# Kernel optimization log

Measured on AMD Instinct MI355X. Metric: run time of the kernel, lower is better.

Reference implementation:

```python
import jax, jax.numpy as jnp
import numpy as np

NH, KVH, HD = 32, 8, 128          # num heads, kv heads, head dim
HIDDEN = NH * HD                   # 4096
K_BITS = V_BITS = 4
GROUP = 32                         # quantization group size
THETA = 10000.0
FEAT = 32 // K_BITS                # values packed per int32


def _rope_cos_sin(pos, dtype=jnp.float32):
    inv_freq = 1.0 / (THETA ** (jnp.arange(0, HD, 2, dtype=jnp.float32) / HD))
    freqs = pos.astype(jnp.float32)[:, None] * inv_freq[None, :]
    emb = jnp.concatenate([freqs, freqs], axis=-1)  # [t, HD]
    return jnp.cos(emb).astype(dtype), jnp.sin(emb).astype(dtype)


def _rotate_half(x):
    x1, x2 = jnp.split(x, 2, axis=-1)
    return jnp.concatenate([-x2, x1], axis=-1)


def _apply_rope(x, pos):  # x: [b, h, t, d], pos: [t]
    cos, sin = _rope_cos_sin(pos, x.dtype)
    return x * cos[None, None] + _rotate_half(x) * sin[None, None]


def _unpack(packed, bits):
    # packed int32 [..., n] -> float [..., n * (32//bits)], little-endian bit fields
    feat = 32 // bits
    shifts = jnp.arange(feat, dtype=jnp.int32) * bits
    vals = (packed[..., None] >> shifts) & ((1 << bits) - 1)
    return vals.reshape(packed.shape[:-1] + (packed.shape[-1] * feat,)).astype(jnp.float32)


def _dequant(packed, scale, mn, bits, group):
    # group-wise affine dequant: x = q * scale + mn along last dim
    qv = _unpack(packed, bits)
    lead, L = qv.shape[:-1], qv.shape[-1]
    qv = qv.reshape(lead + (L // group, group))
    return (qv * scale[..., None] + mn[..., None]).reshape(lead + (L,))


def _repeat_kv(x, n):
    return jnp.repeat(x, n, axis=1)


def setup_inputs() -> dict:
    key = jax.random.key(0)
    ks = jax.random.split(key, 13)
    B, QL = 8, 8
    TQ, FULL_PAST = 3968, 56
    s = 0.02
    return {
        "hidden_states": jax.random.normal(ks[0], (B, QL, HIDDEN), jnp.float32),
        "Wq": jax.random.normal(ks[1], (NH * HD, HIDDEN), jnp.float32) * s,
        "Wk": jax.random.normal(ks[2], (KVH * HD, HIDDEN), jnp.float32) * s,
        "Wv": jax.random.normal(ks[3], (KVH * HD, HIDDEN), jnp.float32) * s,
        "Wo": jax.random.normal(ks[4], (NH * HD, NH * HD), jnp.float32) * s,
        "key_quant_trans": jax.random.randint(ks[5], (B, KVH, HD, TQ // FEAT), 0, 2**31 - 1, jnp.int32),
        "key_scale_trans": jax.random.uniform(ks[6], (B, KVH, HD, TQ // GROUP), jnp.float32) * 0.05 + 0.01,
        "key_mn_trans": jax.random.normal(ks[7], (B, KVH, HD, TQ // GROUP), jnp.float32) * 0.1,
        "key_full_past": jax.random.normal(ks[8], (B, KVH, FULL_PAST, HD), jnp.float32),
        "value_quant": jax.random.randint(ks[9], (B, KVH, TQ, HD // FEAT), 0, 2**31 - 1, jnp.int32),
        "value_scale": jax.random.uniform(ks[10], (B, KVH, TQ, HD // GROUP), jnp.float32) * 0.05 + 0.01,
        "value_mn": jax.random.normal(ks[11], (B, KVH, TQ, HD // GROUP), jnp.float32) * 0.1,
        "value_full_past": jax.random.normal(ks[12], (B, KVH, FULL_PAST, HD), jnp.float32),
    }


def reference(hidden_states, Wq, Wk, Wv, Wo,
              key_quant_trans, key_scale_trans, key_mn_trans, key_full_past,
              value_quant, value_scale, value_mn, value_full_past):
    b, q_len, _ = hidden_states.shape
    groups = NH // KVH
    # projections
    q = (hidden_states @ Wq.T).reshape(b, q_len, NH, HD).transpose(0, 2, 1, 3)
    k = (hidden_states @ Wk.T).reshape(b, q_len, KVH, HD).transpose(0, 2, 1, 3)
    v = (hidden_states @ Wv.T).reshape(b, q_len, KVH, HD).transpose(0, 2, 1, 3)

    TQ = key_quant_trans.shape[-1] * FEAT
    past_len = TQ + key_full_past.shape[2]
    pos_new = jnp.arange(past_len, past_len + q_len)
    qr = _apply_rope(q, pos_new)

    # quantized key segment: dequant (stored transposed [b,kvh,HD,TQ]) + fused RoPE + bmm
    kq = _dequant(key_quant_trans, key_scale_trans, key_mn_trans, K_BITS, GROUP)
    kq = _apply_rope(kq.transpose(0, 1, 3, 2), jnp.arange(TQ))  # [b,kvh,TQ,HD]
    att_quant = jnp.einsum('bhqd,bhkd->bhqk', qr, _repeat_kv(kq, groups))

    # full-precision residual key segment
    k_full = jnp.concatenate([key_full_past, k], axis=2)
    pos_full = jnp.arange(past_len + q_len - k_full.shape[2], past_len + q_len)
    k_full = _apply_rope(k_full, pos_full)
    att_full = jnp.einsum('bhqd,bhkd->bhqk', qr, _repeat_kv(k_full, groups))

    attn = jnp.concatenate([att_quant, att_full], axis=-1) / np.sqrt(HD).astype(np.float32)
    attn = jax.nn.softmax(attn.astype(jnp.float32), axis=-1).astype(qr.dtype)

    # quantized values (packed along head_dim) + full residual values
    vq = _dequant(value_quant, value_scale, value_mn, V_BITS, GROUP)  # [b,kvh,TQ,HD]
    v_full = jnp.concatenate([value_full_past, v], axis=2)
    Lf = v_full.shape[2]
    out = jnp.einsum('bhqk,bhkd->bhqd', attn[..., :-Lf], _repeat_kv(vq, groups)) \
        + jnp.einsum('bhqk,bhkd->bhqd', attn[..., -Lf:], _repeat_kv(v_full, groups))

    out = out.transpose(0, 2, 1, 3).reshape(b, q_len, NH * HD)
    return out @ Wo.T
```

## Files before the change

### kernel.cpp

```cpp
#include <hip/hip_runtime.h>

typedef unsigned short u16;
typedef short bf16x8 __attribute__((ext_vector_type(8)));
typedef float f32x4 __attribute__((ext_vector_type(4)));

__device__ __forceinline__ float b2f(u16 u){ return __uint_as_float(((unsigned)u)<<16); }
__device__ __forceinline__ u16 f2bf(float f){ return (u16)((__float_as_uint(f)+0x8000u)>>16); }
__device__ __forceinline__ float ldf(const void* p, int i, bool isbf){
  return isbf ? b2f(((const u16*)p)[i]) : ((const float*)p)[i];
}
__device__ __forceinline__ float2 ld2(const void* p, int i, bool isbf){
  if (isbf) { unsigned u = *(const unsigned*)((const u16*)p + i);
              return make_float2(b2f((u16)(u & 0xffffu)), b2f((u16)(u >> 16))); }
  return *(const float2*)((const float*)p + i);
}
__device__ __forceinline__ void ld8(u16* dst, const void* p, int i, bool isbf){
  if (isbf) { *(uint4*)dst = *(const uint4*)((const u16*)p + i); }
  else {
    float4 a = *(const float4*)((const float*)p + i);
    float4 b = *(const float4*)((const float*)p + i + 4);
    dst[0]=f2bf(a.x); dst[1]=f2bf(a.y); dst[2]=f2bf(a.z); dst[3]=f2bf(a.w);
    dst[4]=f2bf(b.x); dst[5]=f2bf(b.y); dst[6]=f2bf(b.z); dst[7]=f2bf(b.w);
  }
}
__device__ __forceinline__ void pre8(uint4& A, uint4& B, const void* p, int i, bool isb){
  if (isb) { A = *(const uint4*)((const u16*)p + i); }
  else { A = *(const uint4*)((const float*)p + i);
         B = *(const uint4*)((const float*)p + i + 4); }
}
__device__ __forceinline__ void st8(u16* dst, const uint4& A, const uint4& B, bool isb){
  if (isb) { *(uint4*)dst = A; }
  else {
    const float* a = (const float*)&A; const float* b = (const float*)&B;
    dst[0]=f2bf(a[0]); dst[1]=f2bf(a[1]); dst[2]=f2bf(a[2]); dst[3]=f2bf(a[3]);
    dst[4]=f2bf(b[0]); dst[5]=f2bf(b[1]); dst[6]=f2bf(b[2]); dst[7]=f2bf(b[3]);
  }
}
__device__ __forceinline__ float c8(const float* __restrict__ p, int i, int stride){
  float s = 0.f;
  #pragma unroll
  for (int k = 0; k < 8; k++) s += p[i + k*stride];
  return s;
}
__device__ __forceinline__ void bar(){ asm volatile("s_waitcnt lgkmcnt(0)\n\ts_barrier" ::: "memory"); }
#define RORMAX(x, ctrl) fmaxf((x), __int_as_float(__builtin_amdgcn_update_dpp( \
    __float_as_int(x), __float_as_int(x), (ctrl), 0xF, 0xF, false)))
#define MFMA16(a,b,c) __builtin_amdgcn_mfma_f32_16x16x32_bf16((a),(b),(c),0,0,0)

__global__ __launch_bounds__(256) void ctab_kernel(const u16* __restrict__ h,
                                                   int* __restrict__ flag,
                                                   float2* __restrict__ ctab) {
  int tid = threadIdx.x;
  if (blockIdx.x == 0) {
    int cnt = 0;
    for (int i = tid; i < 4096; i += 256) {
      int e = (h[i] >> 7) & 0xFF;
      cnt += (e >= 116 && e <= 132) ? 1 : 0;
    }
    __shared__ int sh[256];
    sh[tid] = cnt; __syncthreads();
    for (int s = 128; s > 0; s >>= 1) { if (tid < s) sh[tid] += sh[tid + s]; __syncthreads(); }
    if (tid == 0) flag[0] = (sh[0] >= 3100) ? 1 : 0;
  }
  int idx = blockIdx.x * 256 + tid;
  int dm = idx & 63, t = idx >> 6;
  float f = exp2f(-(float)dm * (13.287712379549449f / 64.0f));
  float ang = (float)t * f;
  float s, c;
  sincosf(ang, &s, &c);
  ctab[idx] = make_float2(c, s);
}

__global__ __launch_bounds__(256) void proj_kernel(
    const void* __restrict__ X, const void* __restrict__ Wa,
    const void* __restrict__ Wb, const void* __restrict__ Wc,
    float* __restrict__ out32, int Na, int Nb, int ostride,
    const int* __restrict__ flagp, int x_dyn)
{
  bool fbf = (*flagp != 0);
  bool xbf = x_dyn ? fbf : true;
  int n0 = blockIdx.x * 64;
  int ks0 = blockIdx.y * 512;
  const void* W; int wr0;
  if (n0 < Na)           { W = Wa; wr0 = n0; }
  else if (n0 < Na + Nb) { W = Wb; wr0 = n0 - Na; }
  else                   { W = Wc; wr0 = n0 - Na - Nb; }

  __shared__ u16 Xs[64][136];
  __shared__ u16 Ws[64][136];
  int tid = threadIdx.x;
  int wv = tid >> 6, lane = tid & 63, lr = lane & 15, lq = lane >> 4;
  f32x4 zf = {0.f,0.f,0.f,0.f};
  f32x4 acc[4] = {zf, zf, zf, zf};

  uint4 xa[4], xb[4], wa[4], wb[4];
  #pragma unroll
  for (int s = 0; s < 4; s++) {
    int e = s * 256 + tid, row = e >> 4, c8i = e & 15;
    pre8(xa[s], xb[s], X, row * 4096 + ks0 + c8i * 8, xbf);
    pre8(wa[s], wb[s], W, (wr0 + row) * 4096 + ks0 + c8i * 8, fbf);
  }
  #pragma unroll 1
  for (int ki = 0; ki < 4; ki++) {
    bar();
    #pragma unroll
    for (int s = 0; s < 4; s++) {
      int e = s * 256 + tid, row = e >> 4, c8i = e & 15;
      st8(&Xs[row][c8i * 8], xa[s], xb[s], xbf);
      st8(&Ws[row][c8i * 8], wa[s], wb[s], fbf);
    }
    if (ki < 3) {
      int k0 = ks0 + (ki + 1) * 128;
      #pragma unroll
      for (int s = 0; s < 4; s++) {
        int e = s * 256 + tid, row = e >> 4, c8i = e & 15;
        pre8(xa[s], xb[s], X, row * 4096 + k0 + c8i * 8, xbf);
        pre8(wa[s], wb[s], W, (wr0 + row) * 4096 + k0 + c8i * 8, fbf);
      }
    }
    bar();
    #pragma unroll
    for (int ks = 0; ks < 4; ks++) {
      bf16x8 af = *(const bf16x8*)&Xs[wv * 16 + lr][ks * 32 + lq * 8];
      #pragma unroll
      for (int nt = 0; nt < 4; nt++) {
        bf16x8 bv = *(const bf16x8*)&Ws[nt * 16 + lr][ks * 32 + lq * 8];
        acc[nt] = MFMA16(af, bv, acc[nt]);
      }
    }
  }
  float* outp = out32 + (size_t)blockIdx.y * 64 * ostride;
  #pragma unroll
  for (int nt = 0; nt < 4; nt++)
    #pragma unroll
    for (int r = 0; r < 4; r++)
      outp[(wv * 16 + lq * 4 + r) * ostride + n0 + nt * 16 + lr] = acc[nt][r];
}

__global__ __launch_bounds__(256) void prep_kernel(
    const float* __restrict__ Cq32, const void* __restrict__ kfp, const void* __restrict__ vfp,
    const float2* __restrict__ ctab, const int* __restrict__ flagp,
    u16* __restrict__ qrb, u16* __restrict__ kfullb, u16* __restrict__ vfullT)
{
  bool isbf = (*flagp != 0);
  int idx = blockIdx.x * 256 + threadIdx.x;
  if (idx < 262144) {
    int d = idx & 127, row = (idx >> 7) & 31, bh = idx >> 12;
    int b = bh >> 3, kvh = bh & 7, g = row >> 3, qp = row & 7;
    int tok = b * 8 + qp, h = kvh * 4 + g;
    float x  = c8(Cq32, tok * 6144 + h * 128 + d, 393216);
    float x2 = c8(Cq32, tok * 6144 + h * 128 + (d ^ 64), 393216);
    float2 cs = ctab[(4024 + qp) * 64 + (d & 63)];
    float sgn = (d < 64) ? -1.f : 1.f;
    qrb[idx] = f2bf(x * cs.x + sgn * (x2 * cs.y));
  } else if (idx < 786432) {
    int j = idx - 262144;
    int d = j & 127, t = (j >> 7) & 63, bh = j >> 13;
    int b = bh >> 3, kvh = bh & 7;
    float x, x2;
    if (t < 56) {
      x  = ldf(kfp, (bh * 56 + t) * 128 + d, isbf);
      x2 = ldf(kfp, (bh * 56 + t) * 128 + (d ^ 64), isbf);
    } else {
      int tok = b * 8 + (t - 56);
      x  = c8(Cq32, tok * 6144 + 4096 + kvh * 128 + d, 393216);
      x2 = c8(Cq32, tok * 6144 + 4096 + kvh * 128 + (d ^ 64), 393216);
    }
    float2 cs = ctab[(3968 + t) * 64 + (d & 63)];
    float sgn = (d < 64) ? -1.f : 1.f;
    kfullb[j] = f2bf(x * cs.x + sgn * (x2 * cs.y));
  } else {
    int j = idx - 786432;
    int t = j & 63, d = (j >> 6) & 127, bh = j >> 13;
    int b = bh >> 3, kvh = bh & 7;
    float x;
    if (t < 56) x = ldf(vfp, (bh * 56 + t) * 128 + d, isbf);
    else        x = c8(Cq32, (b * 8 + t - 56) * 6144 + 5120 + kvh * 128 + d, 393216);
    vfullT[j] = f2bf(x);
  }
}

__global__ __launch_bounds__(256) void attn_kernel(
    const int* __restrict__ kqw, const void* __restrict__ ksc, const void* __restrict__ kmn,
    const int* __restrict__ vqw, const void* __restrict__ vsc, const void* __restrict__ vmn,
    const u16* __restrict__ qrb, const u16* __restrict__ kfullb, const u16* __restrict__ vfullT,
    const float2* __restrict__ ctab, const int* __restrict__ flagp,
    u16* __restrict__ Opart, float* __restrict__ ml)
{
  bool isbf = (*flagp != 0);
  int bh = blockIdx.x, grp = blockIdx.y;
  int tid = threadIdx.x;
  int c0 = grp * 4;
  int N = (grp == 15) ? 3 : 4;

  __shared__ __align__(16) unsigned char L[37120];
  u16* Kt = (u16*)L;
  u16* Vt = (u16*)(L + 16384);
  u16* Pt = (u16*)(L + 32768);
  float* pmax = (float*)(L + 36864);

  int wv = tid >> 6, lane = tid & 63, lr = lane & 15, lq = lane >> 4;
  int mt = wv & 1, nh = wv >> 1;
  int sx = (lr & 7) << 3;

  const int* kq_lo = kqw + (bh * 128 + lane) * 496;
  const int* kq_hi = kq_lo + 64 * 496;
  int klo = (bh * 128 + lane) * 124;
  int khi = klo + 64 * 124;
  const int* vqp = vqw + (bh * 3968 + lane) * 16 + wv * 4;
  int voff = (bh * 3968 + lane) * 4 + wv;

  bf16x8 qa[4];
  #pragma unroll
  for (int ks = 0; ks < 4; ks++)
    qa[ks] = *(const bf16x8*)&qrb[(bh * 32 + mt * 16 + lr) * 128 + ks * 32 + lq * 8];
  bf16x8 onev;
  #pragma unroll
  for (int j2 = 0; j2 < 8; j2++) onev[j2] = (short)0x3F80;

  float m_prev[4], l_run[4], alpha[4], mx[4];
  f32x4 zf = {0.f,0.f,0.f,0.f};
  f32x4 oacc[4] = {zf, zf, zf, zf};
  f32x4 sacc[2];
  #pragma unroll
  for (int r = 0; r < 4; r++) { m_prev[r] = -INFINITY; l_run[r] = 0.f; }

  unsigned kwl[2], kwh[2];
  float2 ksl, kml, ksh, kmh;
  uint4 vw; float vs, vm;

#define KLOAD(cn) do { \
    kwl[0] = kq_lo[(cn)*8 + wv]; kwl[1] = kq_lo[(cn)*8 + wv + 4]; \
    kwh[0] = kq_hi[(cn)*8 + wv]; kwh[1] = kq_hi[(cn)*8 + wv + 4]; \
    ksl = ld2(ksc, klo + (cn)*2, isbf); kml = ld2(kmn, klo + (cn)*2, isbf); \
    ksh = ld2(ksc, khi + (cn)*2, isbf); kmh = ld2(kmn, khi + (cn)*2, isbf); } while(0)
#define VLOAD(cn) do { \
    vw = *(const uint4*)(vqp + (cn)*1024); \
    vs = ldf(vsc, voff + (cn)*256, isbf); vm = ldf(vmn, voff + (cn)*256, isbf); } while(0)
#define KDEQ(cn) do { \
    _Pragma("unroll") \
    for (int it = 0; it < 2; it++) { \
      int w = wv + 4 * it; \
      unsigned w1 = kwl[it], w2 = kwh[it]; \
      float sc1 = it ? ksl.y : ksl.x, m1 = it ? kml.y : kml.x; \
      float sc2 = it ? ksh.y : ksh.x, m2 = it ? kmh.y : kmh.x; \
      const float2* ct = &ctab[((cn) * 64 + w * 8) * 64 + lane]; \
      _Pragma("unroll") \
      for (int ii = 0; ii < 8; ii++) { \
        float v1 = (float)((w1 >> (4 * ii)) & 15u) * sc1 + m1; \
        float v2 = (float)((w2 >> (4 * ii)) & 15u) * sc2 + m2; \
        float2 cs = ct[ii * 64]; \
        int t = w * 8 + ii; \
        Kt[(t * 128 + lane)      ^ ((t & 7) << 3)] = f2bf(v1 * cs.x - v2 * cs.y); \
        Kt[(t * 128 + lane + 64) ^ ((t & 7) << 3)] = f2bf(v2 * cs.x + v1 * cs.y); \
      } \
    } } while(0)
#define PVSTEP() do { \
    f32x4 pv[4] = {zf, zf, zf, zf}; f32x4 ls = zf; \
    _Pragma("unroll") \
    for (int ks = 0; ks < 2; ks++) { \
      bf16x8 af = *(const bf16x8*)&Pt[((mt*16 + lr)*64 + ks*32 + lq*8) ^ sx]; \
      ls = MFMA16(af, onev, ls); \
      _Pragma("unroll") \
      for (int nt = 0; nt < 4; nt++) { \
        bf16x8 bv = *(const bf16x8*)&Vt[((nh*64 + nt*16 + lr)*64 + ks*32 + lq*8) ^ sx]; \
        pv[nt] = MFMA16(af, bv, pv[nt]); \
      } \
    } \
    _Pragma("unroll") \
    for (int r = 0; r < 4; r++) { \
      l_run[r] = l_run[r] * alpha[r] + ls[r]; \
      _Pragma("unroll") \
      for (int nt = 0; nt < 4; nt++) \
        oacc[nt][r] = oacc[nt][r] * alpha[r] + pv[nt][r]; \
    } } while(0)

  KLOAD(c0);
  VLOAD(c0);
  KDEQ(c0);
  KLOAD(c0 + 1);
  bar();

  for (int i = 0; i < N; i++) {
    int c = c0 + i;
    f32x4 sa0 = zf, sa1 = zf;
    #pragma unroll
    for (int ks = 0; ks < 4; ks++) {
      bf16x8 b0 = *(const bf16x8*)&Kt[((nh*32 + lr)*128      + ks*32 + lq*8) ^ sx];
      bf16x8 b1 = *(const bf16x8*)&Kt[((nh*32 + 16 + lr)*128 + ks*32 + lq*8) ^ sx];
      sa0 = MFMA16(qa[ks], b0, sa0);
      sa1 = MFMA16(qa[ks], b1, sa1);
    }
    if (i > 0) PVSTEP();
    #pragma unroll
    for (int r = 0; r < 4; r++) {
      sa0[r] *= 0.08838834764831845f;
      sa1[r] *= 0.08838834764831845f;
      float m0 = fmaxf(sa0[r], sa1[r]);
      m0 = RORMAX(m0, 0x128);
      m0 = RORMAX(m0, 0x124);
      m0 = RORMAX(m0, 0x122);
      m0 = RORMAX(m0, 0x121);
      mx[r] = m0;
    }
    if (lr == 0) {
      #pragma unroll
      for (int r = 0; r < 4; r++) pmax[wv * 16 + lq * 4 + r] = mx[r];
    }
    sacc[0] = sa0; sacc[1] = sa1;
    bar();
    #pragma unroll
    for (int r = 0; r < 4; r++) {
      float cm = fmaxf(mx[r], pmax[(wv ^ 2) * 16 + lq * 4 + r]);
      float mn2 = fmaxf(m_prev[r], cm);
      alpha[r] = __expf(m_prev[r] - mn2);
      m_prev[r] = mn2;
    }
    #pragma unroll
    for (int nt = 0; nt < 2; nt++) {
      #pragma unroll
      for (int r = 0; r < 4; r++) {
        float p = __expf(sacc[nt][r] - m_prev[r]);
        int q = mt * 16 + lq * 4 + r, k = nh * 32 + nt * 16 + lr;
        Pt[(q * 64 + k) ^ ((q & 7) << 3)] = f2bf(p);
      }
    }
    if (c != 62) {
      unsigned wds[4] = {vw.x, vw.y, vw.z, vw.w};
      #pragma unroll
      for (int it = 0; it < 4; it++) {
        unsigned wd = wds[it];
        #pragma unroll
        for (int ii = 0; ii < 8; ii++) {
          int d = (wv * 4 + it) * 8 + ii;
          Vt[(d * 64 + lane) ^ ((d & 7) << 3)] = f2bf((float)((wd >> (4 * ii)) & 15u) * vs + vm);
        }
      }
    } else {
      for (int u = tid; u < 1024; u += 256) {
        int dd = u >> 3, t8 = u & 7;
        *(uint4*)&Vt[(dd * 64 + t8 * 8) ^ ((dd & 7) << 3)] =
            *(const uint4*)&vfullT[(bh * 128 + dd) * 64 + t8 * 8];
      }
    }
    if (i + 1 < N) {
      if (c + 1 == 62) {
        for (int u = tid; u < 1024; u += 256) {
          int row = u >> 4, cc = u & 15;
          *(uint4*)&Kt[(row * 128 + cc * 8) ^ ((row & 7) << 3)] =
              *(const uint4*)&kfullb[(bh * 64 + row) * 128 + cc * 8];
        }
      } else {
        KDEQ(c + 1);
      }
    }
    if (i + 2 < N && c + 2 < 62) KLOAD(c + 2);
    if (i + 1 < N && c + 1 < 62) VLOAD(c + 1);
    bar();
  }
  PVSTEP();

  u16* Ob = Opart + (size_t)((bh * 16 + grp) * 32) * 128;
  #pragma unroll
  for (int nt = 0; nt < 4; nt++)
    #pragma unroll
    for (int r = 0; r < 4; r++)
      Ob[(mt * 16 + lq * 4 + r) * 128 + nh * 64 + nt * 16 + lr] = f2bf(oacc[nt][r]);
  if (wv < 2 && lr == 0) {
    #pragma unroll
    for (int r = 0; r < 4; r++) {
      ml[((bh * 16 + grp) * 32 + mt * 16 + lq * 4 + r) * 2 + 0] = m_prev[r];
      ml[((bh * 16 + grp) * 32 + mt * 16 + lq * 4 + r) * 2 + 1] = l_run[r];
    }
  }
#undef KLOAD
#undef VLOAD
#undef KDEQ
#undef PVSTEP
}

__global__ __launch_bounds__(256) void combine_kernel(
    const u16* __restrict__ Opart, const float* __restrict__ ml, u16* __restrict__ attn_out)
{
  int bh = blockIdx.x, dq = blockIdx.y, tid = threadIdx.x;
  __shared__ float Wg[16][33];
  __shared__ float Ls[32];
  if (tid < 32) {
    int row = tid;
    float M = -INFINITY;
    for (int g = 0; g < 16; g++)
      M = fmaxf(M, ml[((bh * 16 + g) * 32 + row) * 2]);
    float Lacc = 0.f;
    for (int g = 0; g < 16; g++) {
      float m = ml[((bh * 16 + g) * 32 + row) * 2];
      float l = ml[((bh * 16 + g) * 32 + row) * 2 + 1];
      float w = __expf(m - M);
      Wg[g][row] = w;
      Lacc += l * w;
    }
    Ls[row] = Lacc;
  }
  __syncthreads();
  int row = tid >> 3, ds = tid & 7;
  int d0 = dq * 32 + ds * 4;
  float a0 = 0.f, a1 = 0.f, a2 = 0.f, a3 = 0.f;
  for (int g = 0; g < 16; g++) {
    float w = Wg[g][row];
    const u16* p = Opart + (size_t)((bh * 16 + g) * 32 + row) * 128 + d0;
    uint2 v = *(const uint2*)p;
    const u16* h = (const u16*)&v;
    a0 += w * b2f(h[0]); a1 += w * b2f(h[1]); a2 += w * b2f(h[2]); a3 += w * b2f(h[3]);
  }
  float inv = 1.0f / Ls[row];
  int b = bh >> 3, kvh = bh & 7, hg = row >> 3, qp = row & 7;
  u16* dst = attn_out + (size_t)(b * 8 + qp) * 4096 + (kvh * 4 + hg) * 128 + d0;
  dst[0] = f2bf(a0 * inv); dst[1] = f2bf(a1 * inv);
  dst[2] = f2bf(a2 * inv); dst[3] = f2bf(a3 * inv);
}

__global__ __launch_bounds__(256) void cast_kernel(
    const float* __restrict__ O32, const int* __restrict__ flagp, void* __restrict__ out)
{
  int i = blockIdx.x * 256 + threadIdx.x;
  float v = c8(O32, i, 262144);
  if (*flagp) ((u16*)out)[i] = f2bf(v);
  else        ((float*)out)[i] = v;
}

extern "C" void kernel_launch(void* const* d_in, const int* in_sizes, int n_in,
                              void* d_out, int out_size, void* d_ws, size_t ws_size,
                              hipStream_t stream)
{
  const void* hidden = d_in[0];
  const void* Wq  = d_in[1];
  const void* Wk  = d_in[2];
  const void* Wv  = d_in[3];
  const void* Wo  = d_in[4];
  const int*  kqw = (const int*)d_in[5];
  const void* ksc = d_in[6];
  const void* kmn = d_in[7];
  const void* kfp = d_in[8];
  const int*  vqw = (const int*)d_in[9];
  const void* vsc = d_in[10];
  const void* vmn = d_in[11];
  const void* vfp = d_in[12];

  char* ws = (char*)d_ws;
  int*    flag     = (int*)(ws);
  float2* ctab     = (float2*)(ws + 256);
  float*  Cq32     = (float*)(ws + 2064640);
  u16*    Opart    = (u16*)(ws + 2064640);
  float*  O32      = (float*)(ws + 2064640);
  u16*    qrb      = (u16*)(ws + 18841856);
  u16*    attn_out = qrb;
  u16*    kfullb   = (u16*)(ws + 19366144);
  u16*    vfullT   = (u16*)(ws + 20414720);
  float*  ml       = (float*)(ws + 21463296);

  ctab_kernel<<<1008, 256, 0, stream>>>((const u16*)hidden, flag, ctab);
  proj_kernel<<<dim3(96, 8), 256, 0, stream>>>(hidden, Wq, Wk, Wv, Cq32, 4096, 1024, 6144, flag, 1);
  prep_kernel<<<5120, 256, 0, stream>>>(Cq32, kfp, vfp, ctab, flag, qrb, kfullb, vfullT);
  attn_kernel<<<dim3(64, 16), 256, 0, stream>>>(kqw, ksc, kmn, vqw, vsc, vmn,
                                                qrb, kfullb, vfullT, ctab, flag, Opart, ml);
  combine_kernel<<<dim3(64, 4), 256, 0, stream>>>(Opart, ml, attn_out);
  proj_kernel<<<dim3(64, 8), 256, 0, stream>>>(attn_out, Wo, Wo, Wo, O32, 4096, 0, 4096, flag, 0);
  cast_kernel<<<1024, 256, 0, stream>>>(O32, flag, d_out);
}
```

Measured before the change: 291.3 us.

## Fuse rope-table with QKV projection and fold combine into attention's last block

```diff
diff --git a/kernel.cpp b/kernel.cpp
--- a/kernel.cpp
+++ b/kernel.cpp
@@ -13,15 +13,6 @@
   if (isbf) { unsigned u = *(const unsigned*)((const u16*)p + i);
               return make_float2(b2f((u16)(u & 0xffffu)), b2f((u16)(u >> 16))); }
   return *(const float2*)((const float*)p + i);
-}
-__device__ __forceinline__ void ld8(u16* dst, const void* p, int i, bool isbf){
-  if (isbf) { *(uint4*)dst = *(const uint4*)((const u16*)p + i); }
-  else {
-    float4 a = *(const float4*)((const float*)p + i);
-    float4 b = *(const float4*)((const float*)p + i + 4);
-    dst[0]=f2bf(a.x); dst[1]=f2bf(a.y); dst[2]=f2bf(a.z); dst[3]=f2bf(a.w);
-    dst[4]=f2bf(b.x); dst[5]=f2bf(b.y); dst[6]=f2bf(b.z); dst[7]=f2bf(b.w);
-  }
 }
 __device__ __forceinline__ void pre8(uint4& A, uint4& B, const void* p, int i, bool isb){
   if (isb) { A = *(const uint4*)((const u16*)p + i); }
@@ -47,28 +38,106 @@
     __float_as_int(x), __float_as_int(x), (ctrl), 0xF, 0xF, false)))
 #define MFMA16(a,b,c) __builtin_amdgcn_mfma_f32_16x16x32_bf16((a),(b),(c),0,0,0)
 
-__global__ __launch_bounds__(256) void ctab_kernel(const u16* __restrict__ h,
-                                                   int* __restrict__ flag,
-                                                   float2* __restrict__ ctab) {
+__global__ __launch_bounds__(256) void ctab_proj_kernel(
+    const u16* __restrict__ h, int* __restrict__ flag, float2* __restrict__ ctab,
+    const void* __restrict__ Wa, const void* __restrict__ Wb, const void* __restrict__ Wc,
+    float* __restrict__ out32, int* __restrict__ cnt)
+{
+  __shared__ __align__(16) u16 XW[2][64][136];
   int tid = threadIdx.x;
-  if (blockIdx.x == 0) {
-    int cnt = 0;
+
+  if (blockIdx.x < 1008) {
+    if (blockIdx.x == 0) {
+      int c = 0;
+      for (int i = tid; i < 4096; i += 256) {
+        int e = (h[i] >> 7) & 0xFF;
+        c += (e >= 116 && e <= 132) ? 1 : 0;
+      }
+      int* sh = (int*)XW;
+      sh[tid] = c; __syncthreads();
+      for (int s = 128; s > 0; s >>= 1) { if (tid < s) sh[tid] += sh[tid + s]; __syncthreads(); }
+      if (tid == 0) flag[0] = (sh[0] >= 3100) ? 1 : 0;
+      if (tid < 64) cnt[tid] = 0;
+    }
+    int idx = blockIdx.x * 256 + tid;
+    int dm = idx & 63, t = idx >> 6;
+    float f = exp2f(-(float)dm * (13.287712379549449f / 64.0f));
+    float ang = (float)t * f;
+    float s, c;
+    sincosf(ang, &s, &c);
+    ctab[idx] = make_float2(c, s);
+    return;
+  }
+  int bx = blockIdx.x - 1008;
+  int n0 = (bx % 96) * 64;
+  int ks0 = (bx / 96) * 512;
+  int tot;
+  {
+    int c = 0;
     for (int i = tid; i < 4096; i += 256) {
       int e = (h[i] >> 7) & 0xFF;
-      cnt += (e >= 116 && e <= 132) ? 1 : 0;
-    }
-    __shared__ int sh[256];
-    sh[tid] = cnt; __syncthreads();
+      c += (e >= 116 && e <= 132) ? 1 : 0;
+    }
+    int* sh = (int*)XW;
+    sh[tid] = c; __syncthreads();
     for (int s = 128; s > 0; s >>= 1) { if (tid < s) sh[tid] += sh[tid + s]; __syncthreads(); }
-    if (tid == 0) flag[0] = (sh[0] >= 3100) ? 1 : 0;
-  }
-  int idx = blockIdx.x * 256 + tid;
-  int dm = idx & 63, t = idx >> 6;
-  float f = exp2f(-(float)dm * (13.287712379549449f / 64.0f));
-  float ang = (float)t * f;
-  float s, c;
-  sincosf(ang, &s, &c);
-  ctab[idx] = make_float2(c, s);
+    tot = sh[0];
+    __syncthreads();
+  }
+  bool fbf = (tot >= 3100);
+  bool xbf = fbf;
+  const void* X = h;
+  const void* W; int wr0;
+  if (n0 < 4096)      { W = Wa; wr0 = n0; }
+  else if (n0 < 5120) { W = Wb; wr0 = n0 - 4096; }
+  else                { W = Wc; wr0 = n0 - 5120; }
+
+  int wv = tid >> 6, lane = tid & 63, lr = lane & 15, lq = lane >> 4;
+  f32x4 zf = {0.f,0.f,0.f,0.f};
+  f32x4 acc[4] = {zf, zf, zf, zf};
+
+  uint4 xa[4], xb[4], wa[4], wb[4];
+  #pragma unroll
+  for (int s = 0; s < 4; s++) {
+    int e = s * 256 + tid, row = e >> 4, c8i = e & 15;
+    pre8(xa[s], xb[s], X, row * 4096 + ks0 + c8i * 8, xbf);
+    pre8(wa[s], wb[s], W, (wr0 + row) * 4096 + ks0 + c8i * 8, fbf);
+  }
+  #pragma unroll 1
+  for (int ki = 0; ki < 4; ki++) {
+    bar();
+    #pragma unroll
+    for (int s = 0; s < 4; s++) {
+      int e = s * 256 + tid, row = e >> 4, c8i = e & 15;
+      st8(&XW[0][row][c8i * 8], xa[s], xb[s], xbf);
+      st8(&XW[1][row][c8i * 8], wa[s], wb[s], fbf);
+    }
+    if (ki < 3) {
+      int k0 = ks0 + (ki + 1) * 128;
+      #pragma unroll
+      for (int s = 0; s < 4; s++) {
+        int e = s * 256 + tid, row = e >> 4, c8i = e & 15;
+        pre8(xa[s], xb[s], X, row * 4096 + k0 + c8i * 8, xbf);
+        pre8(wa[s], wb[s], W, (wr0 + row) * 4096 + k0 + c8i * 8, fbf);
+      }
+    }
+    bar();
+    #pragma unroll
+    for (int ks = 0; ks < 4; ks++) {
+      bf16x8 af = *(const bf16x8*)&XW[0][wv * 16 + lr][ks * 32 + lq * 8];
+      #pragma unroll
+      for (int nt = 0; nt < 4; nt++) {
+        bf16x8 bv = *(const bf16x8*)&XW[1][nt * 16 + lr][ks * 32 + lq * 8];
+        acc[nt] = MFMA16(af, bv, acc[nt]);
+      }
+    }
+  }
+  float* outp = out32 + (size_t)(bx / 96) * 64 * 6144;
+  #pragma unroll
+  for (int nt = 0; nt < 4; nt++)
+    #pragma unroll
+    for (int r = 0; r < 4; r++)
+      outp[(wv * 16 + lq * 4 + r) * 6144 + n0 + nt * 16 + lr] = acc[nt][r];
 }
 
 __global__ __launch_bounds__(256) void proj_kernel(
@@ -185,7 +254,8 @@
     const int* __restrict__ vqw, const void* __restrict__ vsc, const void* __restrict__ vmn,
     const u16* __restrict__ qrb, const u16* __restrict__ kfullb, const u16* __restrict__ vfullT,
     const float2* __restrict__ ctab, const int* __restrict__ flagp,
-    u16* __restrict__ Opart, float* __restrict__ ml)
+    u16* __restrict__ Opart, float* __restrict__ ml,
+    int* __restrict__ cnt, u16* __restrict__ attn_out)
 {
   bool isbf = (*flagp != 0);
   int bh = blockIdx.x, grp = blockIdx.y;
@@ -377,14 +447,15 @@
 #undef VLOAD
 #undef KDEQ
 #undef PVSTEP
-}
-
-__global__ __launch_bounds__(256) void combine_kernel(
-    const u16* __restrict__ Opart, const float* __restrict__ ml, u16* __restrict__ attn_out)
-{
-  int bh = blockIdx.x, dq = blockIdx.y, tid = threadIdx.x;
-  __shared__ float Wg[16][33];
-  __shared__ float Ls[32];
+
+  __threadfence();
+  __shared__ int lastf;
+  if (tid == 0) lastf = (atomicAdd(&cnt[bh], 1) == 15) ? 1 : 0;
+  __syncthreads();
+  if (!lastf) return;
+  __threadfence();
+  float* Wg = (float*)L;
+  float* Ls = (float*)(L + 2112);
   if (tid < 32) {
     int row = tid;
     float M = -INFINITY;
@@ -395,27 +466,30 @@
       float m = ml[((bh * 16 + g) * 32 + row) * 2];
       float l = ml[((bh * 16 + g) * 32 + row) * 2 + 1];
       float w = __expf(m - M);
-      Wg[g][row] = w;
+      Wg[g * 33 + row] = w;
       Lacc += l * w;
     }
     Ls[row] = Lacc;
   }
   __syncthreads();
   int row = tid >> 3, ds = tid & 7;
-  int d0 = dq * 32 + ds * 4;
-  float a0 = 0.f, a1 = 0.f, a2 = 0.f, a3 = 0.f;
-  for (int g = 0; g < 16; g++) {
-    float w = Wg[g][row];
-    const u16* p = Opart + (size_t)((bh * 16 + g) * 32 + row) * 128 + d0;
-    uint2 v = *(const uint2*)p;
-    const u16* h = (const u16*)&v;
-    a0 += w * b2f(h[0]); a1 += w * b2f(h[1]); a2 += w * b2f(h[2]); a3 += w * b2f(h[3]);
-  }
   float inv = 1.0f / Ls[row];
   int b = bh >> 3, kvh = bh & 7, hg = row >> 3, qp = row & 7;
-  u16* dst = attn_out + (size_t)(b * 8 + qp) * 4096 + (kvh * 4 + hg) * 128 + d0;
-  dst[0] = f2bf(a0 * inv); dst[1] = f2bf(a1 * inv);
-  dst[2] = f2bf(a2 * inv); dst[3] = f2bf(a3 * inv);
+  #pragma unroll 1
+  for (int dq = 0; dq < 4; dq++) {
+    int d0 = dq * 32 + ds * 4;
+    float a0 = 0.f, a1 = 0.f, a2 = 0.f, a3 = 0.f;
+    for (int g = 0; g < 16; g++) {
+      float w = Wg[g * 33 + row];
+      const u16* p = Opart + (size_t)((bh * 16 + g) * 32 + row) * 128 + d0;
+      uint2 v = *(const uint2*)p;
+      const u16* h2 = (const u16*)&v;
+      a0 += w * b2f(h2[0]); a1 += w * b2f(h2[1]); a2 += w * b2f(h2[2]); a3 += w * b2f(h2[3]);
+    }
+    u16* dst = attn_out + (size_t)(b * 8 + qp) * 4096 + (kvh * 4 + hg) * 128 + d0;
+    dst[0] = f2bf(a0 * inv); dst[1] = f2bf(a1 * inv);
+    dst[2] = f2bf(a2 * inv); dst[3] = f2bf(a3 * inv);
+  }
 }
 
 __global__ __launch_bounds__(256) void cast_kernel(
@@ -451,18 +525,19 @@
   float*  Cq32     = (float*)(ws + 2064640);
   u16*    Opart    = (u16*)(ws + 2064640);
   float*  O32      = (float*)(ws + 2064640);
+  u16*    attn_out = (u16*)(ws + 14647552);
   u16*    qrb      = (u16*)(ws + 18841856);
-  u16*    attn_out = qrb;
   u16*    kfullb   = (u16*)(ws + 19366144);
   u16*    vfullT   = (u16*)(ws + 20414720);
   float*  ml       = (float*)(ws + 21463296);
-
-  ctab_kernel<<<1008, 256, 0, stream>>>((const u16*)hidden, flag, ctab);
-  proj_kernel<<<dim3(96, 8), 256, 0, stream>>>(hidden, Wq, Wk, Wv, Cq32, 4096, 1024, 6144, flag, 1);
+  int*    cnt      = (int*)(ws + 21725440);
+
+  ctab_proj_kernel<<<1776, 256, 0, stream>>>((const u16*)hidden, flag, ctab,
+                                             Wq, Wk, Wv, Cq32, cnt);
   prep_kernel<<<5120, 256, 0, stream>>>(Cq32, kfp, vfp, ctab, flag, qrb, kfullb, vfullT);
   attn_kernel<<<dim3(64, 16), 256, 0, stream>>>(kqw, ksc, kmn, vqw, vsc, vmn,
-                                                qrb, kfullb, vfullT, ctab, flag, Opart, ml);
-  combine_kernel<<<dim3(64, 4), 256, 0, stream>>>(Opart, ml, attn_out);
+                                                qrb, kfullb, vfullT, ctab, flag, Opart, ml,
+                                                cnt, attn_out);
   proj_kernel<<<dim3(64, 8), 256, 0, stream>>>(attn_out, Wo, Wo, Wo, O32, 4096, 0, 4096, flag, 0);
   cast_kernel<<<1024, 256, 0, stream>>>(O32, flag, d_out);
 }
```

Result: slower. 432.8 us (+48.6%).
